# Optimization experiments

Hardware: AMD Instinct MI355X
Metric: run time of the kernel (lower is better)

Reference implementation:

```python
import jax, jax.numpy as jnp
import numpy as np

D_MODEL = 1024
N_HEADS = 16
HEAD_DIM = D_MODEL // N_HEADS


def setup_inputs() -> dict:
    key = jax.random.key(0)
    ks = jax.random.split(key, 9)
    B, S = 2, 2048
    s = 1.0 / np.sqrt(D_MODEL)
    x = jax.random.normal(ks[0], (B, S, D_MODEL), dtype=jnp.float32)
    Wq = jax.random.normal(ks[1], (N_HEADS, D_MODEL, HEAD_DIM), dtype=jnp.float32) * s
    Wk = jax.random.normal(ks[2], (N_HEADS, D_MODEL, HEAD_DIM), dtype=jnp.float32) * s
    Wv = jax.random.normal(ks[3], (N_HEADS, D_MODEL, HEAD_DIM), dtype=jnp.float32) * s
    bq = jax.random.normal(ks[4], (N_HEADS, HEAD_DIM), dtype=jnp.float32) * s
    bk = jax.random.normal(ks[5], (N_HEADS, HEAD_DIM), dtype=jnp.float32) * s
    bv = jax.random.normal(ks[6], (N_HEADS, HEAD_DIM), dtype=jnp.float32) * s
    Wp = jax.random.normal(ks[7], (D_MODEL, D_MODEL), dtype=jnp.float32) * s
    bp = jax.random.normal(ks[8], (D_MODEL,), dtype=jnp.float32) * s
    return {"x": x, "Wq": Wq, "Wk": Wk, "Wv": Wv, "bq": bq, "bk": bk, "bv": bv, "Wp": Wp, "bp": bp}


def reference(x, Wq, Wk, Wv, bq, bk, bv, Wp, bp):
    # Per-head projections batched over heads: [B,S,D] x [H,D,E] -> [B,H,S,E]
    Q = jnp.einsum('bsd,hde->bhse', x, Wq) + bq[None, :, None, :]
    K = jnp.einsum('bsd,hde->bhse', x, Wk) + bk[None, :, None, :]
    V = jnp.einsum('bsd,hde->bhse', x, Wv) + bv[None, :, None, :]
    scores = jnp.einsum('bhse,bhte->bhst', Q, K) / jnp.sqrt(jnp.asarray(HEAD_DIM, x.dtype))
    attn = jax.nn.softmax(scores, axis=-1)          # [B,H,S,S]
    out = jnp.einsum('bhst,bhte->bhse', attn, V)    # [B,H,S,E]
    B, H, S, E = out.shape
    concat = out.transpose(0, 2, 1, 3).reshape(B, S, H * E)  # concat heads along feature
    return concat @ Wp.T + bp
```

## Files before the change

### kernel.cpp

```cpp
#include <hip/hip_runtime.h>
#include <hip/hip_bf16.h>

typedef __attribute__((ext_vector_type(8))) short short8;
typedef __attribute__((ext_vector_type(4))) float float4_t;

#define D_MODEL 1024
#define N_HEADS 16
#define HEAD_DIM 64
#define B_SZ 2
#define SEQ 2048
#define M_ROWS (B_SZ*SEQ)
#define NQKV 3072
#define SC_LOG2E 0.18033688011112042f

__device__ __forceinline__ unsigned short f2bf(float f) {
  unsigned u = __float_as_uint(f);
  u += 0x7FFFu + ((u >> 16) & 1u);
  return (unsigned short)(u >> 16);
}

__device__ __forceinline__ void gl_lds16(const unsigned short* g, unsigned short* l) {
  __builtin_amdgcn_global_load_lds(
      (const __attribute__((address_space(1))) unsigned int*)(size_t)g,
      (__attribute__((address_space(3))) unsigned int*)(unsigned int)(size_t)l,
      16, 0, 0);
}

__global__ void cvt_bf16(const float* __restrict__ in, unsigned short* __restrict__ out, int n) {
  int i = (blockIdx.x * 256 + threadIdx.x) * 4;
  if (i + 3 < n) {
    float4 v = *(const float4*)(in + i);
    out[i + 0] = f2bf(v.x);
    out[i + 1] = f2bf(v.y);
    out[i + 2] = f2bf(v.z);
    out[i + 3] = f2bf(v.w);
  }
}

__global__ void cvt_wt(const float* __restrict__ in, unsigned short* __restrict__ Wall, int sel) {
  __shared__ float t[16][17];
  int h = blockIdx.z;
  int d0 = blockIdx.x * 16, e0 = blockIdx.y * 16;
  int tx = threadIdx.x & 15, ty = threadIdx.x >> 4;
  t[ty][tx] = in[h * (D_MODEL * HEAD_DIM) + (d0 + ty) * HEAD_DIM + e0 + tx];
  __syncthreads();
  Wall[(size_t)(sel * 1024 + h * 64 + e0 + ty) * D_MODEL + d0 + tx] = f2bf(t[tx][ty]);
}

__global__ __launch_bounds__(256) void qkv_gemm(const unsigned short* __restrict__ xb,
                                                const unsigned short* __restrict__ Wall,
                                                const float* __restrict__ bq,
                                                const float* __restrict__ bk,
                                                const float* __restrict__ bv,
                                                unsigned short* __restrict__ Qb,
                                                unsigned short* __restrict__ Kb,
                                                unsigned short* __restrict__ Vtb) {
  __shared__ unsigned short As[128 * 32], Bs[128 * 32];
  const int m0 = blockIdx.x * 128, n0 = blockIdx.y * 128;
  const int lane = threadIdx.x & 63, w = threadIdx.x >> 6;
  const int l16 = lane & 15, quad = lane >> 4;
  const int wm = w & 1, wn = w >> 1;
  const int ldrow = lane >> 2, ldcol = (lane & 3) * 8;
  const unsigned short* ga0 = xb + (size_t)(m0 + w * 32 + ldrow) * D_MODEL + ldcol;
  const unsigned short* ga1 = ga0 + 16 * D_MODEL;
  const unsigned short* gb0 = Wall + (size_t)(n0 + w * 32 + ldrow) * D_MODEL + ldcol;
  const unsigned short* gb1 = gb0 + 16 * D_MODEL;
  unsigned short* lA0 = As + (w * 2 + 0) * 512;
  unsigned short* lA1 = As + (w * 2 + 1) * 512;
  unsigned short* lB0 = Bs + (w * 2 + 0) * 512;
  unsigned short* lB1 = Bs + (w * 2 + 1) * 512;
  float4_t acc[4][4];
  float4_t z = {0.f, 0.f, 0.f, 0.f};
#pragma unroll
  for (int i = 0; i < 4; i++)
#pragma unroll
    for (int j = 0; j < 4; j++) acc[i][j] = z;
  for (int k0 = 0; k0 < D_MODEL; k0 += 32) {
    __syncthreads();
    gl_lds16(ga0 + k0, lA0);
    gl_lds16(ga1 + k0, lA1);
    gl_lds16(gb0 + k0, lB0);
    gl_lds16(gb1 + k0, lB1);
    __syncthreads();
    short8 af[4], bf[4];
#pragma unroll
    for (int i = 0; i < 4; i++) af[i] = *(const short8*)&As[(wm * 64 + i * 16 + l16) * 32 + quad * 8];
#pragma unroll
    for (int j = 0; j < 4; j++) bf[j] = *(const short8*)&Bs[(wn * 64 + j * 16 + l16) * 32 + quad * 8];
#pragma unroll
    for (int i = 0; i < 4; i++)
#pragma unroll
      for (int j = 0; j < 4; j++)
        acc[i][j] = __builtin_amdgcn_mfma_f32_16x16x32_bf16(af[i], bf[j], acc[i][j], 0, 0, 0);
  }
  const int nb = n0 + wn * 64;
  const int sel = nb >> 10;
  const int h = (nb >> 6) & 15;
  const float* bias = sel == 0 ? bq : (sel == 1 ? bk : bv);
#pragma unroll
  for (int i = 0; i < 4; i++) {
#pragma unroll
    for (int j = 0; j < 4; j++) {
#pragma unroll
      for (int r = 0; r < 4; r++) {
        int m = m0 + wm * 64 + i * 16 + quad * 4 + r;
        int e = j * 16 + l16;
        int bb = m >> 11, s = m & (SEQ - 1);
        size_t bh = (size_t)(bb * N_HEADS + h);
        float v = acc[i][j][r] + bias[h * 64 + e];
        if (sel == 0) {
          Qb[(bh * SEQ + s) * HEAD_DIM + e] = f2bf(v * SC_LOG2E);
        } else if (sel == 1) {
          Kb[(bh * SEQ + s) * HEAD_DIM + e] = f2bf(v);
        } else {
          Vtb[bh * (32 * 4096) + (size_t)(s >> 6) * 4096 + e * 64 + (s & 63)] = f2bf(v);
        }
      }
    }
  }
}

__global__ __launch_bounds__(256) void attn_kernel(const unsigned short* __restrict__ Q,
                                                   const unsigned short* __restrict__ K,
                                                   const unsigned short* __restrict__ Vt,
                                                   unsigned short* __restrict__ concat) {
  __shared__ __align__(16) unsigned short Ks[2][64 * 72];
  __shared__ __align__(16) unsigned short Vs[2][64 * 72];
  __shared__ __align__(16) unsigned short Ps[4][32 * 72];
  const int b = blockIdx.z, h = blockIdx.y;
  const int lane = threadIdx.x & 63, w = threadIdx.x >> 6;
  const int l16 = lane & 15, quad = lane >> 4;
  const size_t bh = (size_t)(b * N_HEADS + h);
  const int q0 = blockIdx.x * 128 + w * 32;
  float4_t z = {0.f, 0.f, 0.f, 0.f};

  short8 aq[2][2];
#pragma unroll
  for (int rg = 0; rg < 2; rg++)
#pragma unroll
    for (int hf = 0; hf < 2; hf++)
      aq[rg][hf] = *(const short8*)(Q + (bh * SEQ + q0 + rg * 16 + l16) * HEAD_DIM + hf * 32 + quad * 8);

  const int srow = lane >> 3;
  const int schk = lane & 7;
  const unsigned short* kg0 = K + (bh * SEQ + w * 16 + srow) * HEAD_DIM + schk * 8;
  const unsigned short* kg1 = kg0 + 8 * HEAD_DIM;
  const unsigned short* vg0 = Vt + bh * (32 * 4096) + (w * 16 + srow) * 64 + schk * 8;
  const unsigned short* vg1 = vg0 + 8 * 64;
  const int tl0 = w * 16 + srow, tl1 = tl0 + 8;
  const int kr0 = ((tl0 >> 1) & 15) | ((tl0 & 1) << 4) | (tl0 & 32);
  const int kr1 = ((tl1 >> 1) & 15) | ((tl1 & 1) << 4) | (tl1 & 32);
  const int vr0 = w * 16 + srow, vr1 = vr0 + 8;

  float4_t o[2][4];
  float4_t ls[2] = {z, z};
#pragma unroll
  for (int rg = 0; rg < 2; rg++)
#pragma unroll
    for (int ne = 0; ne < 4; ne++) o[rg][ne] = z;
  short8 ones;
#pragma unroll
  for (int i = 0; i < 8; i++) ones[i] = (short)0x3F80;

  unsigned short* pb = &Ps[w][0];

  short8 kreg0 = *(const short8*)kg0;
  short8 kreg1 = *(const short8*)kg1;
  short8 vreg0 = *(const short8*)vg0;
  short8 vreg1 = *(const short8*)vg1;

  for (int it = 0; it < 32; ++it) {
    unsigned short* kb = &Ks[it & 1][0];
    unsigned short* vb = &Vs[it & 1][0];
    *(short8*)(kb + kr0 * 72 + schk * 8) = kreg0;
    *(short8*)(kb + kr1 * 72 + schk * 8) = kreg1;
    *(short8*)(vb + vr0 * 72 + schk * 8) = vreg0;
    *(short8*)(vb + vr1 * 72 + schk * 8) = vreg1;
    __syncthreads();
    if (it < 31) {
      size_t go = (size_t)(it + 1) * 4096;
      kreg0 = *(const short8*)(kg0 + go);
      kreg1 = *(const short8*)(kg1 + go);
      vreg0 = *(const short8*)(vg0 + go);
      vreg1 = *(const short8*)(vg1 + go);
    }
    float4_t s[2][4];
#pragma unroll
    for (int nt = 0; nt < 4; nt++) {
      short8 k0 = *(const short8*)(kb + (nt * 16 + l16) * 72 + quad * 8);
      short8 k1 = *(const short8*)(kb + (nt * 16 + l16) * 72 + 32 + quad * 8);
      s[0][nt] = __builtin_amdgcn_mfma_f32_16x16x32_bf16(aq[0][0], k0, z, 0, 0, 0);
      s[0][nt] = __builtin_amdgcn_mfma_f32_16x16x32_bf16(aq[0][1], k1, s[0][nt], 0, 0, 0);
      s[1][nt] = __builtin_amdgcn_mfma_f32_16x16x32_bf16(aq[1][0], k0, z, 0, 0, 0);
      s[1][nt] = __builtin_amdgcn_mfma_f32_16x16x32_bf16(aq[1][1], k1, s[1][nt], 0, 0, 0);
    }
#pragma unroll
    for (int rg = 0; rg < 2; rg++) {
#pragma unroll
      for (int r = 0; r < 4; r++) {
        int row = rg * 16 + quad * 4 + r;
        float p0 = __builtin_amdgcn_exp2f(s[rg][0][r]);
        float p1 = __builtin_amdgcn_exp2f(s[rg][1][r]);
        __hip_bfloat162 pp = __float22bfloat162_rn(float2{p0, p1});
        *(unsigned int*)(pb + row * 72 + 2 * l16) = *(unsigned int*)&pp;
        float p2 = __builtin_amdgcn_exp2f(s[rg][2][r]);
        float p3 = __builtin_amdgcn_exp2f(s[rg][3][r]);
        __hip_bfloat162 qq = __float22bfloat162_rn(float2{p2, p3});
        *(unsigned int*)(pb + row * 72 + 32 + 2 * l16) = *(unsigned int*)&qq;
      }
    }
    short8 pa[2][2];
#pragma unroll
    for (int rg = 0; rg < 2; rg++)
#pragma unroll
      for (int hf = 0; hf < 2; hf++)
        pa[rg][hf] = *(const short8*)(pb + (rg * 16 + l16) * 72 + hf * 32 + quad * 8);
#pragma unroll
    for (int rg = 0; rg < 2; rg++) {
      ls[rg] = __builtin_amdgcn_mfma_f32_16x16x32_bf16(pa[rg][0], ones, ls[rg], 0, 0, 0);
      ls[rg] = __builtin_amdgcn_mfma_f32_16x16x32_bf16(pa[rg][1], ones, ls[rg], 0, 0, 0);
    }
#pragma unroll
    for (int ne = 0; ne < 4; ne++) {
#pragma unroll
      for (int hf = 0; hf < 2; hf++) {
        short8 vf = *(const short8*)(vb + (ne * 16 + l16) * 72 + hf * 32 + quad * 8);
        o[0][ne] = __builtin_amdgcn_mfma_f32_16x16x32_bf16(pa[0][hf], vf, o[0][ne], 0, 0, 0);
        o[1][ne] = __builtin_amdgcn_mfma_f32_16x16x32_bf16(pa[1][hf], vf, o[1][ne], 0, 0, 0);
      }
    }
  }
#pragma unroll
  for (int rg = 0; rg < 2; rg++) {
#pragma unroll
    for (int r = 0; r < 4; r++) {
      float li = 1.0f / ls[rg][r];
      int sr = q0 + rg * 16 + quad * 4 + r;
#pragma unroll
      for (int ne = 0; ne < 4; ne++)
        concat[((size_t)(b * SEQ + sr)) * D_MODEL + h * 64 + ne * 16 + l16] = f2bf(o[rg][ne][r] * li);
    }
  }
}

__global__ __launch_bounds__(256) void out_gemm(const unsigned short* __restrict__ cb,
                                                const unsigned short* __restrict__ Wpb,
                                                const float* __restrict__ bp,
                                                float* __restrict__ out) {
  __shared__ unsigned short As[128 * 32], Bs[128 * 32];
  const int m0 = blockIdx.x * 128, n0 = blockIdx.y * 128;
  const int lane = threadIdx.x & 63, w = threadIdx.x >> 6;
  const int l16 = lane & 15, quad = lane >> 4;
  const int wm = w & 1, wn = w >> 1;
  const int ldrow = lane >> 2, ldcol = (lane & 3) * 8;
  const unsigned short* ga0 = cb + (size_t)(m0 + w * 32 + ldrow) * D_MODEL + ldcol;
  const unsigned short* ga1 = ga0 + 16 * D_MODEL;
  const unsigned short* gb0 = Wpb + (size_t)(n0 + w * 32 + ldrow) * D_MODEL + ldcol;
  const unsigned short* gb1 = gb0 + 16 * D_MODEL;
  unsigned short* lA0 = As + (w * 2 + 0) * 512;
  unsigned short* lA1 = As + (w * 2 + 1) * 512;
  unsigned short* lB0 = Bs + (w * 2 + 0) * 512;
  unsigned short* lB1 = Bs + (w * 2 + 1) * 512;
  float4_t acc[4][4];
  float4_t z = {0.f, 0.f, 0.f, 0.f};
#pragma unroll
  for (int i = 0; i < 4; i++)
#pragma unroll
    for (int j = 0; j < 4; j++) acc[i][j] = z;
  for (int k0 = 0; k0 < D_MODEL; k0 += 32) {
    __syncthreads();
    gl_lds16(ga0 + k0, lA0);
    gl_lds16(ga1 + k0, lA1);
    gl_lds16(gb0 + k0, lB0);
    gl_lds16(gb1 + k0, lB1);
    __syncthreads();
    short8 af[4], bf[4];
#pragma unroll
    for (int i = 0; i < 4; i++) af[i] = *(const short8*)&As[(wm * 64 + i * 16 + l16) * 32 + quad * 8];
#pragma unroll
    for (int j = 0; j < 4; j++) bf[j] = *(const short8*)&Bs[(wn * 64 + j * 16 + l16) * 32 + quad * 8];
#pragma unroll
    for (int i = 0; i < 4; i++)
#pragma unroll
      for (int j = 0; j < 4; j++)
        acc[i][j] = __builtin_amdgcn_mfma_f32_16x16x32_bf16(af[i], bf[j], acc[i][j], 0, 0, 0);
  }
#pragma unroll
  for (int i = 0; i < 4; i++)
#pragma unroll
    for (int j = 0; j < 4; j++)
#pragma unroll
      for (int r = 0; r < 4; r++) {
        int m = m0 + wm * 64 + i * 16 + quad * 4 + r;
        int oc = n0 + wn * 64 + j * 16 + l16;
        out[(size_t)m * D_MODEL + oc] = acc[i][j][r] + bp[oc];
      }
}

extern "C" void kernel_launch(void* const* d_in, const int* in_sizes, int n_in,
                              void* d_out, int out_size, void* d_ws, size_t ws_size,
                              hipStream_t stream) {
  const float* x  = (const float*)d_in[0];
  const float* Wq = (const float*)d_in[1];
  const float* Wk = (const float*)d_in[2];
  const float* Wv = (const float*)d_in[3];
  const float* bq = (const float*)d_in[4];
  const float* bk = (const float*)d_in[5];
  const float* bv = (const float*)d_in[6];
  const float* Wp = (const float*)d_in[7];
  const float* bp = (const float*)d_in[8];
  float* out = (float*)d_out;

  char* ws = (char*)d_ws;
  size_t off = 0;
  auto alloc = [&](size_t bytes) -> void* {
    void* p = ws + off;
    off += (bytes + 255) & ~(size_t)255;
    return p;
  };
  unsigned short* xb   = (unsigned short*)alloc((size_t)M_ROWS * D_MODEL * 2);
  unsigned short* Wall = (unsigned short*)alloc((size_t)NQKV * D_MODEL * 2);
  unsigned short* Wpb  = (unsigned short*)alloc((size_t)D_MODEL * D_MODEL * 2);
  unsigned short* Qb   = (unsigned short*)alloc((size_t)B_SZ * N_HEADS * SEQ * HEAD_DIM * 2);
  unsigned short* Kb   = (unsigned short*)alloc((size_t)B_SZ * N_HEADS * SEQ * HEAD_DIM * 2);
  unsigned short* Vtb  = (unsigned short*)alloc((size_t)B_SZ * N_HEADS * SEQ * HEAD_DIM * 2);
  unsigned short* cbuf = (unsigned short*)alloc((size_t)B_SZ * SEQ * D_MODEL * 2);

  cvt_bf16<<<(M_ROWS * D_MODEL) / 1024, 256, 0, stream>>>(x, xb, M_ROWS * D_MODEL);
  cvt_bf16<<<(D_MODEL * D_MODEL) / 1024, 256, 0, stream>>>(Wp, Wpb, D_MODEL * D_MODEL);
  cvt_wt<<<dim3(D_MODEL / 16, HEAD_DIM / 16, N_HEADS), 256, 0, stream>>>(Wq, Wall, 0);
  cvt_wt<<<dim3(D_MODEL / 16, HEAD_DIM / 16, N_HEADS), 256, 0, stream>>>(Wk, Wall, 1);
  cvt_wt<<<dim3(D_MODEL / 16, HEAD_DIM / 16, N_HEADS), 256, 0, stream>>>(Wv, Wall, 2);

  qkv_gemm<<<dim3(M_ROWS / 128, NQKV / 128), 256, 0, stream>>>(xb, Wall, bq, bk, bv, Qb, Kb, Vtb);

  attn_kernel<<<dim3(SEQ / 128, N_HEADS, B_SZ), 256, 0, stream>>>(Qb, Kb, Vtb, cbuf);

  out_gemm<<<dim3(M_ROWS / 128, D_MODEL / 128), 256, 0, stream>>>(cbuf, Wpb, bp, out);
}
```

Measured before the change: 215.6 us.

## Fuse conversion kernels, stage V transpose via LDS, unroll attention double-buffer

```diff
diff --git a/kernel.cpp b/kernel.cpp
--- a/kernel.cpp
+++ b/kernel.cpp
@@ -26,25 +26,33 @@
       16, 0, 0);
 }
 
-__global__ void cvt_bf16(const float* __restrict__ in, unsigned short* __restrict__ out, int n) {
-  int i = (blockIdx.x * 256 + threadIdx.x) * 4;
-  if (i + 3 < n) {
-    float4 v = *(const float4*)(in + i);
-    out[i + 0] = f2bf(v.x);
-    out[i + 1] = f2bf(v.y);
-    out[i + 2] = f2bf(v.z);
-    out[i + 3] = f2bf(v.w);
-  }
-}
-
-__global__ void cvt_wt(const float* __restrict__ in, unsigned short* __restrict__ Wall, int sel) {
+__global__ void prep(const float* __restrict__ x, const float* __restrict__ Wp,
+                     const float* __restrict__ Wq, const float* __restrict__ Wk,
+                     const float* __restrict__ Wv,
+                     unsigned short* __restrict__ xb, unsigned short* __restrict__ Wpb,
+                     unsigned short* __restrict__ Wall) {
   __shared__ float t[16][17];
-  int h = blockIdx.z;
-  int d0 = blockIdx.x * 16, e0 = blockIdx.y * 16;
-  int tx = threadIdx.x & 15, ty = threadIdx.x >> 4;
-  t[ty][tx] = in[h * (D_MODEL * HEAD_DIM) + (d0 + ty) * HEAD_DIM + e0 + tx];
-  __syncthreads();
-  Wall[(size_t)(sel * 1024 + h * 64 + e0 + ty) * D_MODEL + d0 + tx] = f2bf(t[tx][ty]);
+  int bid = blockIdx.x;
+  if (bid < 5120) {
+    const float* src; unsigned short* dst; int base;
+    if (bid < 4096) { src = x;  dst = xb;  base = bid * 1024 + threadIdx.x * 4; }
+    else            { src = Wp; dst = Wpb; base = (bid - 4096) * 1024 + threadIdx.x * 4; }
+    float4 v = *(const float4*)(src + base);
+    dst[base + 0] = f2bf(v.x);
+    dst[base + 1] = f2bf(v.y);
+    dst[base + 2] = f2bf(v.z);
+    dst[base + 3] = f2bf(v.w);
+  } else {
+    int u = bid - 5120;
+    int sel = u >> 12;
+    u &= 4095;
+    const float* W = sel == 0 ? Wq : (sel == 1 ? Wk : Wv);
+    int d0 = (u & 63) * 16, e0 = ((u >> 6) & 3) * 16, hh = u >> 8;
+    int tx = threadIdx.x & 15, ty = threadIdx.x >> 4;
+    t[ty][tx] = W[hh * (D_MODEL * HEAD_DIM) + (d0 + ty) * HEAD_DIM + e0 + tx];
+    __syncthreads();
+    Wall[(size_t)(sel * 1024 + hh * 64 + e0 + ty) * D_MODEL + d0 + tx] = f2bf(t[tx][ty]);
+  }
 }
 
 __global__ __launch_bounds__(256) void qkv_gemm(const unsigned short* __restrict__ xb,
@@ -56,6 +64,7 @@
                                                 unsigned short* __restrict__ Kb,
                                                 unsigned short* __restrict__ Vtb) {
   __shared__ unsigned short As[128 * 32], Bs[128 * 32];
+  __shared__ __align__(16) unsigned short Vstage[4][16 * 72];
   const int m0 = blockIdx.x * 128, n0 = blockIdx.y * 128;
   const int lane = threadIdx.x & 63, w = threadIdx.x >> 6;
   const int l16 = lane & 15, quad = lane >> 4;
@@ -97,23 +106,42 @@
   const int sel = nb >> 10;
   const int h = (nb >> 6) & 15;
   const float* bias = sel == 0 ? bq : (sel == 1 ? bk : bv);
-#pragma unroll
-  for (int i = 0; i < 4; i++) {
+  if (sel == 2) {
+    unsigned short* vs = &Vstage[w][0];
+    const int mbase = m0 + wm * 64;
+    const int bb = mbase >> 11;
+    const size_t vbase = (size_t)(bb * N_HEADS + h) * (32 * 4096) +
+                         (size_t)((mbase >> 6) & 31) * 4096;
+    const int e8 = lane >> 3, ch = lane & 7;
 #pragma unroll
     for (int j = 0; j < 4; j++) {
-#pragma unroll
-      for (int r = 0; r < 4; r++) {
-        int m = m0 + wm * 64 + i * 16 + quad * 4 + r;
-        int e = j * 16 + l16;
-        int bb = m >> 11, s = m & (SEQ - 1);
-        size_t bh = (size_t)(bb * N_HEADS + h);
-        float v = acc[i][j][r] + bias[h * 64 + e];
-        if (sel == 0) {
-          Qb[(bh * SEQ + s) * HEAD_DIM + e] = f2bf(v * SC_LOG2E);
-        } else if (sel == 1) {
-          Kb[(bh * SEQ + s) * HEAD_DIM + e] = f2bf(v);
-        } else {
-          Vtb[bh * (32 * 4096) + (size_t)(s >> 6) * 4096 + e * 64 + (s & 63)] = f2bf(v);
+      float be = bias[h * 64 + j * 16 + l16];
+#pragma unroll
+      for (int i = 0; i < 4; i++)
+#pragma unroll
+        for (int r = 0; r < 4; r++)
+          vs[l16 * 72 + i * 16 + quad * 4 + r] = f2bf(acc[i][j][r] + be);
+#pragma unroll
+      for (int rd = 0; rd < 2; rd++) {
+        int er = rd * 8 + e8;
+        short8 val = *(const short8*)(vs + er * 72 + ch * 8);
+        *(short8*)(Vtb + vbase + (size_t)(j * 16 + er) * 64 + ch * 8) = val;
+      }
+    }
+  } else {
+#pragma unroll
+    for (int i = 0; i < 4; i++) {
+#pragma unroll
+      for (int j = 0; j < 4; j++) {
+#pragma unroll
+        for (int r = 0; r < 4; r++) {
+          int m = m0 + wm * 64 + i * 16 + quad * 4 + r;
+          int e = j * 16 + l16;
+          int bb = m >> 11, s = m & (SEQ - 1);
+          size_t bh = (size_t)(bb * N_HEADS + h);
+          float v = acc[i][j][r] + bias[h * 64 + e];
+          if (sel == 0) Qb[(bh * SEQ + s) * HEAD_DIM + e] = f2bf(v * SC_LOG2E);
+          else          Kb[(bh * SEQ + s) * HEAD_DIM + e] = f2bf(v);
         }
       }
     }
@@ -124,8 +152,8 @@
                                                    const unsigned short* __restrict__ K,
                                                    const unsigned short* __restrict__ Vt,
                                                    unsigned short* __restrict__ concat) {
-  __shared__ __align__(16) unsigned short Ks[2][64 * 72];
-  __shared__ __align__(16) unsigned short Vs[2][64 * 72];
+  __shared__ __align__(16) unsigned short Ks0[64 * 72], Ks1[64 * 72];
+  __shared__ __align__(16) unsigned short Vs0[64 * 72], Vs1[64 * 72];
   __shared__ __align__(16) unsigned short Ps[4][32 * 72];
   const int b = blockIdx.z, h = blockIdx.y;
   const int lane = threadIdx.x & 63, w = threadIdx.x >> 6;
@@ -141,16 +169,14 @@
     for (int hf = 0; hf < 2; hf++)
       aq[rg][hf] = *(const short8*)(Q + (bh * SEQ + q0 + rg * 16 + l16) * HEAD_DIM + hf * 32 + quad * 8);
 
-  const int srow = lane >> 3;
-  const int schk = lane & 7;
-  const unsigned short* kg0 = K + (bh * SEQ + w * 16 + srow) * HEAD_DIM + schk * 8;
-  const unsigned short* kg1 = kg0 + 8 * HEAD_DIM;
-  const unsigned short* vg0 = Vt + bh * (32 * 4096) + (w * 16 + srow) * 64 + schk * 8;
-  const unsigned short* vg1 = vg0 + 8 * 64;
+  const int srow = lane >> 3, schk = lane & 7;
+  const unsigned short* kg = K + (bh * SEQ + w * 16 + srow) * HEAD_DIM + schk * 8;
+  const unsigned short* vg = Vt + bh * (32 * 4096) + (w * 16 + srow) * 64 + schk * 8;
   const int tl0 = w * 16 + srow, tl1 = tl0 + 8;
-  const int kr0 = ((tl0 >> 1) & 15) | ((tl0 & 1) << 4) | (tl0 & 32);
-  const int kr1 = ((tl1 >> 1) & 15) | ((tl1 & 1) << 4) | (tl1 & 32);
-  const int vr0 = w * 16 + srow, vr1 = vr0 + 8;
+  const int kwr0 = (((tl0 >> 1) & 15) | ((tl0 & 1) << 4) | (tl0 & 32)) * 72 + schk * 8;
+  const int kwr1 = (((tl1 >> 1) & 15) | ((tl1 & 1) << 4) | (tl1 & 32)) * 72 + schk * 8;
+  const int vwr0 = (w * 16 + srow) * 72 + schk * 8;
+  const int vwr1 = vwr0 + 8 * 72;
 
   float4_t o[2][4];
   float4_t ls[2] = {z, z};
@@ -161,28 +187,26 @@
   short8 ones;
 #pragma unroll
   for (int i = 0; i < 8; i++) ones[i] = (short)0x3F80;
-
   unsigned short* pb = &Ps[w][0];
 
-  short8 kreg0 = *(const short8*)kg0;
-  short8 kreg1 = *(const short8*)kg1;
-  short8 vreg0 = *(const short8*)vg0;
-  short8 vreg1 = *(const short8*)vg1;
-
-  for (int it = 0; it < 32; ++it) {
-    unsigned short* kb = &Ks[it & 1][0];
-    unsigned short* vb = &Vs[it & 1][0];
-    *(short8*)(kb + kr0 * 72 + schk * 8) = kreg0;
-    *(short8*)(kb + kr1 * 72 + schk * 8) = kreg1;
-    *(short8*)(vb + vr0 * 72 + schk * 8) = vreg0;
-    *(short8*)(vb + vr1 * 72 + schk * 8) = vreg1;
-    __syncthreads();
-    if (it < 31) {
-      size_t go = (size_t)(it + 1) * 4096;
-      kreg0 = *(const short8*)(kg0 + go);
-      kreg1 = *(const short8*)(kg1 + go);
-      vreg0 = *(const short8*)(vg0 + go);
-      vreg1 = *(const short8*)(vg1 + go);
+  short8 kreg0 = *(const short8*)kg;
+  short8 kreg1 = *(const short8*)(kg + 512);
+  short8 vreg0 = *(const short8*)vg;
+  short8 vreg1 = *(const short8*)(vg + 512);
+  kg += 4096; vg += 4096;
+
+  auto step = [&](unsigned short* kb, unsigned short* vb, int itv) {
+    *(short8*)(kb + kwr0) = kreg0;
+    *(short8*)(kb + kwr1) = kreg1;
+    *(short8*)(vb + vwr0) = vreg0;
+    *(short8*)(vb + vwr1) = vreg1;
+    __syncthreads();
+    if (itv < 31) {
+      kreg0 = *(const short8*)kg;
+      kreg1 = *(const short8*)(kg + 512);
+      vreg0 = *(const short8*)vg;
+      vreg1 = *(const short8*)(vg + 512);
+      kg += 4096; vg += 4096;
     }
     float4_t s[2][4];
 #pragma unroll
@@ -229,7 +253,13 @@
         o[1][ne] = __builtin_amdgcn_mfma_f32_16x16x32_bf16(pa[1][hf], vf, o[1][ne], 0, 0, 0);
       }
     }
-  }
+  };
+
+  for (int it2 = 0; it2 < 16; ++it2) {
+    step(Ks0, Vs0, 2 * it2);
+    step(Ks1, Vs1, 2 * it2 + 1);
+  }
+
 #pragma unroll
   for (int rg = 0; rg < 2; rg++) {
 #pragma unroll
@@ -326,11 +356,7 @@
   unsigned short* Vtb  = (unsigned short*)alloc((size_t)B_SZ * N_HEADS * SEQ * HEAD_DIM * 2);
   unsigned short* cbuf = (unsigned short*)alloc((size_t)B_SZ * SEQ * D_MODEL * 2);
 
-  cvt_bf16<<<(M_ROWS * D_MODEL) / 1024, 256, 0, stream>>>(x, xb, M_ROWS * D_MODEL);
-  cvt_bf16<<<(D_MODEL * D_MODEL) / 1024, 256, 0, stream>>>(Wp, Wpb, D_MODEL * D_MODEL);
-  cvt_wt<<<dim3(D_MODEL / 16, HEAD_DIM / 16, N_HEADS), 256, 0, stream>>>(Wq, Wall, 0);
-  cvt_wt<<<dim3(D_MODEL / 16, HEAD_DIM / 16, N_HEADS), 256, 0, stream>>>(Wk, Wall, 1);
-  cvt_wt<<<dim3(D_MODEL / 16, HEAD_DIM / 16, N_HEADS), 256, 0, stream>>>(Wv, Wall, 2);
+  prep<<<17408, 256, 0, stream>>>(x, Wp, Wq, Wk, Wv, xb, Wpb, Wall);
 
   qkv_gemm<<<dim3(M_ROWS / 128, NQKV / 128), 256, 0, stream>>>(xb, Wall, bq, bk, bv, Qb, Kb, Vtb);
 
```

Measured after the change: 207.3 us. 1.04x faster.
